# Kernel optimization log

Measured on AMD Instinct MI355X. Metric: run time of the kernel, lower is better.

The kernel has to match this reference:

```python
import jax, jax.numpy as jnp
import numpy as np

N_PRED = 10000
N_GT = 1000
NUM_CLASSES = 80
IMG_H = 800
IMG_W = 1333
EPS = 1e-12
ALPHA, GAMMA, CLS_W = 0.25, 2.0, 2.0
L1_W, IOU_W = 5.0, 2.0
CENTER_RADIUS = 2.5
CAND_TOPK = 5


def _make_boxes(key, n, w, h):
    k1, k2 = jax.random.split(key)
    cxcy = jax.random.uniform(k1, (n, 2)) * jnp.array([w, h], jnp.float32)
    wh = jax.random.uniform(k2, (n, 2)) * 190.0 + 10.0
    return jnp.concatenate([cxcy - wh / 2, cxcy + wh / 2], axis=1).astype(jnp.float32)


def setup_inputs() -> dict:
    key = jax.random.key(0)
    k1, k2, k3, k4 = jax.random.split(key, 4)
    return {
        'pred_logits': jax.random.normal(k1, (N_PRED, NUM_CLASSES), jnp.float32),
        'pred_boxes': _make_boxes(k2, N_PRED, IMG_W, IMG_H),
        'gt_bboxes': _make_boxes(k3, N_GT, IMG_W, IMG_H),
        'gt_labels': jax.random.randint(k4, (N_GT,), 0, NUM_CLASSES),
        'img_h': IMG_H,
        'img_w': IMG_W,
    }


def _pairwise_iou_giou(pred, gt):
    area_p = (pred[:, 2] - pred[:, 0]) * (pred[:, 3] - pred[:, 1])
    area_g = (gt[:, 2] - gt[:, 0]) * (gt[:, 3] - gt[:, 1])
    lt = jnp.maximum(pred[:, None, :2], gt[None, :, :2])
    rb = jnp.minimum(pred[:, None, 2:], gt[None, :, 2:])
    wh = jnp.clip(rb - lt, 0.0)
    inter = wh[..., 0] * wh[..., 1]                       # [N,G]
    union = area_p[:, None] + area_g[None, :] - inter
    iou = inter / jnp.maximum(union, EPS)
    elt = jnp.minimum(pred[:, None, :2], gt[None, :, :2])
    erb = jnp.maximum(pred[:, None, 2:], gt[None, :, 2:])
    ewh = jnp.clip(erb - elt, 0.0)
    enclose = ewh[..., 0] * ewh[..., 1]
    giou = iou - (enclose - union) / jnp.maximum(enclose, EPS)
    return iou, giou


def _center_info(pred, gt):
    # pred/gt in xyxy; uses pred box centers, strict inequalities as in source
    pcx = (pred[:, 0] + pred[:, 2]) * 0.5
    pcy = (pred[:, 1] + pred[:, 3]) * 0.5
    gx1, gy1, gx2, gy2 = gt[:, 0], gt[:, 1], gt[:, 2], gt[:, 3]
    in_boxes = ((pcx[:, None] > gx1) & (pcx[:, None] < gx2) &
                (pcy[:, None] > gy1) & (pcy[:, None] < gy2))
    gcx, gcy = (gx1 + gx2) * 0.5, (gy1 + gy2) * 0.5
    gw, gh = gx2 - gx1, gy2 - gy1
    r = CENTER_RADIUS
    in_centers = ((pcx[:, None] > gcx - r * gw) & (pcx[:, None] < gcx + r * gw) &
                  (pcy[:, None] > gcy - r * gh) & (pcy[:, None] < gcy + r * gh))
    valid = in_boxes.any(1) | in_centers.any(1)
    return valid, in_boxes & in_centers


def _compute_cost_and_ious(pred_logits, pred_boxes, gt_bboxes, gt_labels, img_h, img_w):
    # FocalLossCost
    p = jax.nn.sigmoid(pred_logits)
    neg = -jnp.log1p(-(p - EPS)) * (1 - ALPHA) * p ** GAMMA
    pos = -jnp.log(p + EPS) * ALPHA * (1 - p) ** GAMMA
    cls_cost = (pos - neg)[:, gt_labels] * CLS_W            # [N,G]
    # BBoxL1Cost (normalized by image size)
    factor = jnp.array([img_w, img_h, img_w, img_h], jnp.float32)
    l1_cost = jnp.sum(jnp.abs(pred_boxes[:, None, :] / factor -
                              gt_bboxes[None, :, :] / factor), -1) * L1_W
    # IoUCost (giou) + pairwise ious for dynamic-k
    ious, giou = _pairwise_iou_giou(pred_boxes, gt_bboxes)
    iou_cost = -giou * IOU_W
    valid_mask, in_boxes_and_center = _center_info(pred_boxes, gt_bboxes)
    cost = cls_cost + l1_cost + iou_cost + jnp.where(in_boxes_and_center, 0.0, 100.0)
    cost = cost + jnp.where(valid_mask, 0.0, 10000.0)[:, None]
    return cost, ious


def _dynamic_k_matching(cost, ious):
    n, g = cost.shape
    k = min(CAND_TOPK, n)
    topk_ious, _ = jax.lax.top_k(ious.T, k)                 # [G,k]
    dynamic_ks = jnp.maximum(topk_ious.sum(1).astype(jnp.int32), 1)
    _, idx = jax.lax.top_k(-cost.T, k)                      # [G,k] smallest costs per gt
    vals = (jnp.arange(k)[None, :] < dynamic_ks[:, None]).astype(cost.dtype)
    cols = jnp.broadcast_to(jnp.arange(g)[:, None], (g, k))
    mm = jnp.zeros_like(cost).at[idx, cols].max(vals)       # scatter 1s per gt column
    # resolve priors matched to >1 gt (note: mask is reused stale inside the loop, as in source)
    prior_mask = mm.sum(1) > 1
    cmin = jnp.argmin(cost, axis=1)
    mm = jnp.where(prior_mask[:, None], jax.nn.one_hot(cmin, g, dtype=cost.dtype), mm)

    def cond(state):
        m, _ = state
        return jnp.any(m.sum(0) == 0)

    def body(state):
        m, c = state
        matched_q = m.sum(1) > 0
        c = c + 100000.0 * matched_q[:, None].astype(c.dtype)
        unmatched = m.sum(0) == 0
        pos = jnp.argmin(c, axis=0)                         # [G]
        oh = jax.nn.one_hot(pos, n, dtype=c.dtype).T        # [N,G]
        m = jnp.where(unmatched[None, :], oh, m)
        cmin2 = jnp.argmin(c, axis=1)
        m_fix = jnp.where(prior_mask[:, None], jax.nn.one_hot(cmin2, g, dtype=c.dtype), m)
        m = jnp.where(jnp.any(m.sum(1) > 1), m_fix, m)
        return (m, c)

    mm, _ = jax.lax.while_loop(cond, body, (mm, cost))
    fg_mask = mm.sum(1) > 0
    matched = jnp.argmax(mm, axis=1).astype(jnp.int32)
    return fg_mask, jnp.where(fg_mask, matched, 0)


def reference(pred_logits, pred_boxes, gt_bboxes, gt_labels, img_h, img_w):
    cost, ious = _compute_cost_and_ious(pred_logits, pred_boxes, gt_bboxes,
                                        gt_labels, img_h, img_w)
    fg_mask, matched_gt = _dynamic_k_matching(cost, ious)
    # dense form: matched_gt[i] valid only where fg_mask[i] (fixed-shape version of
    # the original's compressed matched_gt_inds = mm[fg_mask].argmax(1))
    return fg_mask, matched_gt
```

## Files before the change

### kernel.cpp

```cpp
#include <hip/hip_runtime.h>
#include <cfloat>
#include <cmath>

#define NP 10000
#define NG 1000
#define NC 80
#define LMAX 6
#define NCH 2
#define CHSZ (NP / NCH)
#define MAIN_IT 19
#define TAIL_N  136

#define S_MULTI 12
#define S_BODY  16
#define RI_BIG  0x3fffffff
#define KMAX    0xFFFFFFFFFFFFFFFFull

#define TKEY    0xC248000000000000ull
#define CAND_CAP 1536

__device__ __forceinline__ bool lexless(float av, int ai, float bv, int bi) {
    return (av < bv) || (av == bv && ai < bi);
}

__device__ __forceinline__ unsigned long long packkey(float v, int idx) {
    unsigned u = __float_as_uint(v);
    u ^= (unsigned)(((int)u) >> 31) | 0x80000000u;
    return ((unsigned long long)u << 32) | (unsigned)idx;
}
__device__ __forceinline__ int keyidx(unsigned long long k) {
    return (int)(unsigned)(k & 0xFFFFFFFFu);
}

__device__ __forceinline__ float inflate(float c, int k) {
    for (int q = 0; q < k; q++) c += 100000.0f;
    return c;
}

__device__ __forceinline__ void cost_iou(float4 p, float4 pn, float4 pi,
        float4 g, float4 cb, float4 Gn, float ga, float clsv,
        float& cc_out, float& iou_out) {
#pragma clang fp contract(off)
    float wx = fminf(p.z, g.z) - fmaxf(p.x, g.x); wx = fmaxf(wx, 0.0f);
    float wy = fminf(p.w, g.w) - fmaxf(p.y, g.y); wy = fmaxf(wy, 0.0f);
    float inter = wx * wy;
    float uni = pi.z + ga - inter;
    float iou = inter / fmaxf(uni, 1e-12f);
    float ex = fmaxf(p.z, g.z) - fminf(p.x, g.x); ex = fmaxf(ex, 0.0f);
    float ey = fmaxf(p.w, g.w) - fminf(p.y, g.y); ey = fmaxf(ey, 0.0f);
    float enc = ex * ey;
    float giou = iou - (enc - uni) / fmaxf(enc, 1e-12f);
    float l1 = ((fabsf(pn.x - Gn.x) + fabsf(pn.y - Gn.y))
                + fabsf(pn.z - Gn.z)) + fabsf(pn.w - Gn.w);
    float cc = clsv + l1 * 5.0f;
    cc = cc + (-giou * 2.0f);
    bool inb = (pi.x > g.x && pi.x < g.z && pi.y > g.y && pi.y < g.w);
    bool inc = (pi.x > cb.x && pi.x < cb.z && pi.y > cb.y && pi.y < cb.w);
    cc = cc + ((inb && inc) ? 0.0f : 100.0f);
    cc = cc + pi.w;
    cc_out = cc; iou_out = iou;
}

#define CLS_TI 64
#define PB_CLS0 40
#define PB_G0   197
#define PB_V0   201
__global__ __launch_bounds__(256) void k_prep(const float* __restrict__ logits,
        const float* __restrict__ pb, const float* __restrict__ gb,
        const int* __restrict__ imgw, const int* __restrict__ imgh,
        float* __restrict__ clsval, float4* __restrict__ pnorm,
        float4* __restrict__ pinfo, float4* __restrict__ gcb,
        float4* __restrict__ gnm, float* __restrict__ gar,
        int* rowcnt, int* rowfirst, int* rowiter, int* prior, int* priorcol,
        int* colsum, int* scal)
{
    __shared__ float sl[CLS_TI * (NC + 1)];
    int b = blockIdx.x;
    if (b < PB_CLS0) {
        int i = b * 256 + threadIdx.x;
        if (i < NP) {
            rowcnt[i] = 0; rowfirst[i] = 0x7fffffff; rowiter[i] = RI_BIG;
            prior[i] = 0; priorcol[i] = 0;
        }
        if (i < NG) colsum[i] = 0;
        if (i < 32) scal[i] = 0;
    } else if (b < PB_G0) {
        int i0 = (b - PB_CLS0) * CLS_TI;
        bool full = (i0 + CLS_TI) <= NP;
        if (full) {
            const float* src = logits + (size_t)i0 * NC;
            for (int e = threadIdx.x; e < CLS_TI * NC; e += 256) {
                int di = e / NC, c = e - di * NC;
                sl[di * (NC + 1) + c] = src[e];
            }
        } else {
            for (int e = threadIdx.x; e < CLS_TI * NC; e += 256) {
                int di = e / NC, c = e - di * NC;
                int i = i0 + di;
                sl[di * (NC + 1) + c] = (i < NP) ? logits[(size_t)i * NC + c] : 0.0f;
            }
        }
        __syncthreads();
        for (int e = threadIdx.x; e < CLS_TI * NC; e += 256) {
            int c = e >> 6, di = e & 63;
            int i = i0 + di;
            if (i >= NP) continue;
            float x = sl[di * (NC + 1) + c];
            float p = 1.0f / (1.0f + expf(-x));
            float neg = -log1pf(-(p - 1e-12f)) * 0.75f * (p * p);
            float om = 1.0f - p;
            float pos = -logf(p + 1e-12f) * 0.25f * (om * om);
            clsval[(size_t)c * NP + i] = (pos - neg) * 2.0f;
        }
    } else if (b < PB_V0) {
#pragma clang fp contract(off)
        int j = (b - PB_G0) * 256 + threadIdx.x;
        if (j < NG) {
            float fw = (float)imgw[0], fh = (float)imgh[0];
            float4 g = ((const float4*)gb)[j];
            float gcx = (g.x + g.z) * 0.5f, gcy = (g.y + g.w) * 0.5f;
            float gw = g.z - g.x, gh = g.w - g.y;
            float4 cb; cb.x = gcx - 2.5f * gw; cb.y = gcy - 2.5f * gh;
            cb.z = gcx + 2.5f * gw; cb.w = gcy + 2.5f * gh;
            gcb[j] = cb;
            float4 Gn; Gn.x = g.x / fw; Gn.y = g.y / fh; Gn.z = g.z / fw; Gn.w = g.w / fh;
            gnm[j] = Gn;
            gar[j] = (g.z - g.x) * (g.w - g.y);
        }
    } else {
#pragma clang fp contract(off)
        int wave = threadIdx.x >> 6;
        int lane = threadIdx.x & 63;
        int i = (b - PB_V0) * 4 + wave;
        if (i >= NP) return;
        float4 p = ((const float4*)pb)[i];
        float pcx = (p.x + p.z) * 0.5f, pcy = (p.y + p.w) * 0.5f;
        int vb = 0, vc = 0;
        const float4* gb4 = (const float4*)gb;
        for (int jb = 0; jb < NG; jb += 64) {
            int j = jb + lane;
            if (j < NG) {
                float4 g = gb4[j];
                vb |= (pcx > g.x && pcx < g.z && pcy > g.y && pcy < g.w) ? 1 : 0;
                float gcx = (g.x + g.z) * 0.5f, gcy = (g.y + g.w) * 0.5f;
                float gw = g.z - g.x, gh = g.w - g.y;
                vc |= (pcx > gcx - 2.5f * gw && pcx < gcx + 2.5f * gw &&
                       pcy > gcy - 2.5f * gh && pcy < gcy + 2.5f * gh) ? 1 : 0;
            }
            if (__any(vb | vc)) break;
        }
        int any = __any(vb | vc) ? 1 : 0;
        if (lane == 0) {
            float fw = (float)imgw[0], fh = (float)imgh[0];
            float4 pn; pn.x = p.x / fw; pn.y = p.y / fh; pn.z = p.z / fw; pn.w = p.w / fh;
            pnorm[i] = pn;
            float4 pi4; pi4.x = pcx; pi4.y = pcy;
            pi4.z = (p.z - p.x) * (p.w - p.y);
            pi4.w = any ? 0.0f : 10000.0f;
            pinfo[i] = pi4;
        }
    }
}

__device__ __forceinline__ void upd2(unsigned long long& k0,
        unsigned long long& k1, unsigned long long key) {
    unsigned long long mx = (k0 > key) ? k0 : key;
    k0 = (k0 > key) ? key : k0;
    k1 = (k1 > mx) ? mx : k1;
}
__device__ __forceinline__ void updi2(float& i0, float& i1, float iou) {
    float mnv = fminf(i0, iou);
    i0 = fmaxf(i0, iou);
    i1 = fmaxf(i1, mnv);
}

__global__ __launch_bounds__(256) void k_cost2(
        const float* __restrict__ pb, const float* __restrict__ gb,
        const int* __restrict__ glab, const float* __restrict__ clsval,
        const float4* __restrict__ pnorm, const float4* __restrict__ pinfo,
        const float4* __restrict__ gcb, const float4* __restrict__ gnm,
        const float* __restrict__ gar,
        unsigned long long* __restrict__ pck, float* __restrict__ piv)
{
    __shared__ unsigned long long s_k[256 * 7];
    __shared__ float s_iv[256 * 7];
    __shared__ int s_bad;
    __shared__ int s_cnt;
    int* s_list = (int*)s_iv;

    int j = blockIdx.x >> 1;
    int c = blockIdx.x & 1;
    int tid = threadIdx.x;
    if (tid == 0) { s_bad = 0; s_cnt = 0; }
    float4 g  = ((const float4*)gb)[j];
    float4 cb = gcb[j];
    float4 Gn = gnm[j];
    float  ga = gar[j];
    const float* clscol = clsval + (size_t)glab[j] * NP;
    const float4* pb4 = (const float4*)pb;
    int base_i = c * CHSZ;
    __syncthreads();

    for (int k = 0; k <= MAIN_IT; k++) {
        if (k == MAIN_IT && tid >= TAIL_N) break;
        int i = base_i + tid + k * 256;
        float4 p = pb4[i];
        bool o = (p.z > g.x) & (g.z > p.x) & (p.w > g.y) & (g.w > p.y);
        unsigned long long m = __ballot(o ? 1 : 0);
        if (m) {
            int ln = tid & 63;
            int basew = 0;
            if (ln == 0) basew = atomicAdd(&s_cnt, __popcll(m));
            basew = __shfl(basew, 0);
            if (o) {
                int slot = basew + __popcll(m & ((1ull << ln) - 1ull));
                if (slot < CAND_CAP) s_list[slot] = i;
            }
        }
    }
    __syncthreads();
    int cnt = s_cnt;
    bool overflow = (cnt > CAND_CAP);
    if (overflow) cnt = 0;

    unsigned long long k0 = KMAX, k1 = KMAX;
    float i0 = 0.0f, i1 = 0.0f;
    for (int q = tid; q < cnt; q += 256) {
        int i = s_list[q];
        float cc, iou;
        cost_iou(pb4[i], pnorm[i], pinfo[i], g, cb, Gn, ga, clscol[i], cc, iou);
        upd2(k0, k1, packkey(cc, i));
        updi2(i0, i1, iou);
    }
    __syncthreads();

    int base = tid * 7;
    s_k[base+0] = k0; s_k[base+1] = k1;
    s_k[base+2] = KMAX; s_k[base+3] = KMAX; s_k[base+4] = KMAX; s_k[base+5] = KMAX;
    s_iv[base+0] = i0; s_iv[base+1] = i1;
    s_iv[base+2] = 0.0f; s_iv[base+3] = 0.0f; s_iv[base+4] = 0.0f; s_iv[base+5] = 0.0f;
    __syncthreads();

    for (int w = 128; w > 0; w >>= 1) {
        if (tid < w) {
            int a = tid * 7, bb = (tid + w) * 7;
            unsigned long long ok[5]; float og[5];
            int pa = a, pbp = bb;
#pragma unroll
            for (int t = 0; t < 5; t++) {
                unsigned long long A = s_k[pa], B = s_k[pbp];
                if (A <= B) { ok[t] = A; pa++; } else { ok[t] = B; pbp++; }
            }
            int qa = a, qb = bb;
#pragma unroll
            for (int t = 0; t < 5; t++) {
                float A = s_iv[qa], B = s_iv[qb];
                if (A >= B) { og[t] = A; qa++; } else { og[t] = B; qb++; }
            }
#pragma unroll
            for (int t = 0; t < 5; t++) { s_k[a+t] = ok[t]; s_iv[a+t] = og[t]; }
        }
        __syncthreads();
    }

    if (overflow || s_k[4] >= TKEY || k1 < s_k[4] || i1 > s_iv[4]) s_bad = 1;
    __syncthreads();

    if (s_bad) {
        unsigned long long kv[5]; float iv[5];
#pragma unroll
        for (int t = 0; t < 5; t++) { kv[t] = KMAX; iv[t] = -1.0f; }
        for (int k = 0; k <= MAIN_IT; k++) {
            if (k == MAIN_IT && tid >= TAIL_N) break;
            int i = base_i + tid + k * 256;
            float cc, iou;
            cost_iou(pb4[i], pnorm[i], pinfo[i], g, cb, Gn, ga, clscol[i], cc, iou);
            unsigned long long key = packkey(cc, i);
            if (key < kv[4]) {
                kv[4] = key;
#pragma unroll
                for (int t = 4; t > 0; t--)
                    if (kv[t] < kv[t-1]) { unsigned long long tv = kv[t]; kv[t] = kv[t-1]; kv[t-1] = tv; }
            }
            if (iou > iv[4]) {
                iv[4] = iou;
#pragma unroll
                for (int t = 4; t > 0; t--)
                    if (iv[t] > iv[t-1]) { float tv = iv[t]; iv[t] = iv[t-1]; iv[t-1] = tv; }
            }
        }
#pragma unroll
        for (int t = 0; t < 5; t++) { s_k[base+t] = kv[t]; s_iv[base+t] = iv[t]; }
        s_k[base+5] = KMAX; s_iv[base+5] = -2.0f;
        __syncthreads();
        for (int w = 128; w > 0; w >>= 1) {
            if (tid < w) {
                int a = tid * 7, bb = (tid + w) * 7;
                unsigned long long ok[5]; float og[5];
                int pa = a, pbp = bb;
#pragma unroll
                for (int t = 0; t < 5; t++) {
                    unsigned long long A = s_k[pa], B = s_k[pbp];
                    if (A <= B) { ok[t] = A; pa++; } else { ok[t] = B; pbp++; }
                }
                int qa = a, qb = bb;
#pragma unroll
                for (int t = 0; t < 5; t++) {
                    float A = s_iv[qa], B = s_iv[qb];
                    if (A >= B) { og[t] = A; qa++; } else { og[t] = B; qb++; }
                }
#pragma unroll
                for (int t = 0; t < 5; t++) { s_k[a+t] = ok[t]; s_iv[a+t] = og[t]; }
            }
            __syncthreads();
        }
    }

    if (tid == 0) {
        int ob = blockIdx.x * 5;
#pragma unroll
        for (int t = 0; t < 5; t++) { pck[ob + t] = s_k[t]; piv[ob + t] = s_iv[t]; }
    }
}

__global__ __launch_bounds__(256) void k_costmerge(
        const unsigned long long* __restrict__ pck, const float* __restrict__ piv,
        int* __restrict__ rowcnt, int* __restrict__ rowfirst,
        int* __restrict__ rowiter, int* __restrict__ top5,
        int* __restrict__ dkarr)
{
    int j = blockIdx.x * 256 + threadIdx.x;
    if (j >= NG) return;
    int base = j * 2 * 5;
    int h0 = 0, h1 = 0;
    int besti[5];
#pragma unroll
    for (int r = 0; r < 5; r++) {
        unsigned long long v0 = pck[base + h0];
        unsigned long long v1 = pck[base + 5 + h1];
        if (v0 <= v1) { besti[r] = keyidx(v0); h0++; }
        else          { besti[r] = keyidx(v1); h1++; }
    }
    int g0 = 0, g1 = 0;
    float ivm[5];
#pragma unroll
    for (int r = 0; r < 5; r++) {
        float v0 = piv[base + g0];
        float v1 = piv[base + 5 + g1];
        if (v0 >= v1) { ivm[r] = v0; g0++; } else { ivm[r] = v1; g1++; }
    }
    float s = (((ivm[0] + ivm[1]) + ivm[2]) + ivm[3]) + ivm[4];
    int dk = (int)s;
    if (dk < 1) dk = 1;
    dkarr[j] = dk;
#pragma unroll
    for (int r = 0; r < 5; r++) top5[j * 5 + r] = besti[r];
    for (int t = 0; t < dk; t++) {
        int r = besti[t];
        atomicAdd(&rowcnt[r], 1);
        atomicMin(&rowfirst[r], j);
        atomicMin(&rowiter[r], -1);
    }
}

__global__ __launch_bounds__(256) void k_pfixsurv(const float* __restrict__ pb,
        const float* __restrict__ gb, const int* __restrict__ glab,
        const float* __restrict__ clsval,
        const float4* __restrict__ pnorm, const float4* __restrict__ pinfo,
        const float4* __restrict__ gcb, const float4* __restrict__ gnm,
        const float* __restrict__ gar,
        int* __restrict__ prior, int* __restrict__ priorcol,
        int* __restrict__ colsum,
        const int* __restrict__ rowcnt, const int* __restrict__ top5,
        const int* __restrict__ dkarr)
{
    int b = blockIdx.x;
    int tid = threadIdx.x;
    if (b >= 2500) {
        int j = (b - 2500) * 256 + tid;
        if (j >= NG) return;
        int c = 0;
        int dk = dkarr[j];
        for (int t = 0; t < dk; t++) if (rowcnt[top5[j * 5 + t]] == 1) c++;
        if (c) atomicAdd(&colsum[j], c);
        return;
    }
    __shared__ float rv[256]; __shared__ int ri[256];
    for (int q = 0; q < 4; q++) {
        int row = b * 4 + q;
        if (rowcnt[row] <= 1) continue;
        if (tid == 0) prior[row] = 1;
        float4 p = ((const float4*)pb)[row];
        float4 pn = pnorm[row];
        float4 pi4 = pinfo[row];
        float best = FLT_MAX; int bj = 0x7fffffff;
        for (int j = tid; j < NG; j += 256) {
            float cc, iou;
            cost_iou(p, pn, pi4, ((const float4*)gb)[j], gcb[j], gnm[j], gar[j],
                     clsval[(size_t)glab[j] * NP + row], cc, iou);
            if (lexless(cc, j, best, bj)) { best = cc; bj = j; }
        }
        rv[tid] = best; ri[tid] = bj; __syncthreads();
        for (int w = 128; w > 0; w >>= 1) {
            if (tid < w) {
                float ov = rv[tid + w]; int oi = ri[tid + w];
                if (lexless(ov, oi, rv[tid], ri[tid])) { rv[tid] = ov; ri[tid] = oi; }
            }
            __syncthreads();
        }
        if (tid == 0) {
            priorcol[row] = ri[0];
            atomicAdd(&colsum[ri[0]], 1);
        }
        __syncthreads();
    }
}

__global__ __launch_bounds__(256) void k_iterB(const float* __restrict__ pb,
        const float* __restrict__ gb, const int* __restrict__ glab,
        const float* __restrict__ clsval,
        const float4* __restrict__ pnorm, const float4* __restrict__ pinfo,
        const float4* __restrict__ gcb, const float4* __restrict__ gnm,
        const float* __restrict__ gar, const int* __restrict__ top5,
        int* __restrict__ rowiter, int* __restrict__ rowcnt,
        int* __restrict__ rowfirst, int* __restrict__ colsum,
        int* __restrict__ scal, int t)
{
    int j = blockIdx.x;
    if (colsum[j] != 0) return;
    int tid = threadIdx.x;
    if (tid == 0) scal[S_BODY + t] = 1;

    __shared__ int s_pos;
    if (tid == 0) {
        int pos = -1;
        for (int r = 0; r < 5; r++) {
            int i = top5[j * 5 + r];
            if (rowiter[i] >= t) { pos = i; break; }
        }
        s_pos = pos;
    }
    __syncthreads();
    int pos = s_pos;

    if (pos < 0) {
        float4 g  = ((const float4*)gb)[j];
        float4 cb = gcb[j];
        float4 Gn = gnm[j];
        float  ga = gar[j];
        const float* clscol = clsval + (size_t)glab[j] * NP;
        const float4* pb4 = (const float4*)pb;
        __shared__ float rv[256]; __shared__ int ri[256];
        float best = FLT_MAX; int bi = 0x7fffffff;
        for (int i = tid; i < NP; i += 256) {
            if (rowiter[i] < t) continue;
            float cc, iou;
            cost_iou(pb4[i], pnorm[i], pinfo[i], g, cb, Gn, ga, clscol[i], cc, iou);
            if (lexless(cc, i, best, bi)) { best = cc; bi = i; }
        }
        rv[tid] = best; ri[tid] = bi; __syncthreads();
        for (int w = 128; w > 0; w >>= 1) {
            if (tid < w) {
                float ov = rv[tid + w]; int oi = ri[tid + w];
                if (lexless(ov, oi, rv[tid], ri[tid])) { rv[tid] = ov; ri[tid] = oi; }
            }
            __syncthreads();
        }
        pos = ri[0];
    }

    if (tid == 0) {
        colsum[j] = 1;
        int old = atomicAdd(&rowcnt[pos], 1);
        if (old >= 1) scal[S_MULTI] = 1;
        atomicMin(&rowfirst[pos], j);
        atomicMin(&rowiter[pos], t);
    }
}

__global__ __launch_bounds__(256) void k_iterC(const float* __restrict__ pb,
        const float* __restrict__ gb, const int* __restrict__ glab,
        const float* __restrict__ clsval,
        const float4* __restrict__ pnorm, const float4* __restrict__ pinfo,
        const float4* __restrict__ gcb, const float4* __restrict__ gnm,
        const float* __restrict__ gar,
        const int* __restrict__ prior, const int* __restrict__ rowiter,
        int* __restrict__ priorcol, int* __restrict__ colsum,
        int* __restrict__ scal, int t)
{
    if (scal[S_BODY + t] == 0 || scal[S_MULTI] == 0) return;
    int b = blockIdx.x;
    int tid = threadIdx.x;
    __shared__ float rv[256]; __shared__ int ri[256];
    for (int q = 0; q < 4; q++) {
        int row = b * 4 + q;
        if (!prior[row]) continue;
        int k = t - rowiter[row]; if (k < 0) k = 0;
        float4 p = ((const float4*)pb)[row];
        float4 pn = pnorm[row];
        float4 pi4 = pinfo[row];
        float best = FLT_MAX; int bj = 0x7fffffff;
        for (int j = tid; j < NG; j += 256) {
            float cc, iou;
            cost_iou(p, pn, pi4, ((const float4*)gb)[j], gcb[j], gnm[j], gar[j],
                     clsval[(size_t)glab[j] * NP + row], cc, iou);
            float val = inflate(cc, k);
            if (lexless(val, j, best, bj)) { best = val; bj = j; }
        }
        rv[tid] = best; ri[tid] = bj; __syncthreads();
        for (int w = 128; w > 0; w >>= 1) {
            if (tid < w) {
                float ov = rv[tid + w]; int oi = ri[tid + w];
                if (lexless(ov, oi, rv[tid], ri[tid])) { rv[tid] = ov; ri[tid] = oi; }
            }
            __syncthreads();
        }
        if (tid == 0) {
            int nb = ri[0];
            int oldc = priorcol[row];
            if (nb != oldc) {
                atomicSub(&colsum[oldc], 1);
                atomicAdd(&colsum[nb], 1);
                priorcol[row] = nb;
            }
        }
        __syncthreads();
    }
}

__global__ __launch_bounds__(256) void k_final(const int* __restrict__ rowcnt,
        const int* __restrict__ prior, const int* __restrict__ priorcol,
        const int* __restrict__ rowfirst, int* __restrict__ out)
{
    int i = blockIdx.x * 256 + threadIdx.x;
    if (i >= NP) return;
    int fg = rowcnt[i] > 0;
    out[i] = fg ? 1 : 0;
    out[NP + i] = fg ? (prior[i] ? priorcol[i] : rowfirst[i]) : 0;
}

extern "C" void kernel_launch(void* const* d_in, const int* in_sizes, int n_in,
                              void* d_out, int out_size, void* d_ws, size_t ws_size,
                              hipStream_t stream)
{
    (void)in_sizes; (void)n_in; (void)out_size; (void)ws_size;
    const float* logits = (const float*)d_in[0];
    const float* pboxes = (const float*)d_in[1];
    const float* gboxes = (const float*)d_in[2];
    const int*   glab   = (const int*)d_in[3];
    const int*   imgh   = (const int*)d_in[4];
    const int*   imgw   = (const int*)d_in[5];
    int* out = (int*)d_out;

    char* w = (char*)d_ws;
    float*  clsval  = (float*)(w);
    float4* pnorm   = (float4*)(w + 3200000);
    float4* pinfo   = (float4*)(w + 3360000);
    float4* gcb     = (float4*)(w + 3520000);
    float4* gnm     = (float4*)(w + 3536000);
    float*  gar     = (float*)(w + 3552000);
    int* rowcnt     = (int*)(w + 3556000);
    int* rowfirst   = (int*)(w + 3596000);
    int* rowiter    = (int*)(w + 3636000);
    int* prior      = (int*)(w + 3676000);
    int* priorcol   = (int*)(w + 3716000);
    int* top5       = (int*)(w + 3756000);
    int* dkarr      = (int*)(w + 3776000);
    int* colsum     = (int*)(w + 3780000);
    int* scal       = (int*)(w + 3784000);
    unsigned long long* pck = (unsigned long long*)(w + 3784128);
    float* piv      = (float*)(w + 3864128);

    hipLaunchKernelGGL(k_prep, dim3(2701), dim3(256), 0, stream,
                       logits, pboxes, gboxes, imgw, imgh,
                       clsval, pnorm, pinfo, gcb, gnm, gar,
                       rowcnt, rowfirst, rowiter, prior, priorcol, colsum, scal);
    hipLaunchKernelGGL(k_cost2, dim3(NG * NCH), dim3(256), 0, stream,
                       pboxes, gboxes, glab, clsval, pnorm, pinfo, gcb, gnm, gar,
                       pck, piv);
    hipLaunchKernelGGL(k_costmerge, dim3(4), dim3(256), 0, stream,
                       pck, piv, rowcnt, rowfirst, rowiter, top5, dkarr);
    hipLaunchKernelGGL(k_pfixsurv, dim3(2504), dim3(256), 0, stream,
                       pboxes, gboxes, glab, clsval, pnorm, pinfo, gcb, gnm, gar,
                       prior, priorcol, colsum, rowcnt, top5, dkarr);
    for (int t = 0; t < LMAX; t++) {
        hipLaunchKernelGGL(k_iterB, dim3(NG), dim3(256), 0, stream,
                           pboxes, gboxes, glab, clsval, pnorm, pinfo, gcb, gnm, gar,
                           top5, rowiter, rowcnt, rowfirst, colsum, scal, t);
        hipLaunchKernelGGL(k_iterC, dim3(2500), dim3(256), 0, stream,
                           pboxes, gboxes, glab, clsval, pnorm, pinfo, gcb, gnm, gar,
                           prior, rowiter, priorcol, colsum, scal, t);
    }
    hipLaunchKernelGGL(k_final, dim3(40), dim3(256), 0, stream,
                       rowcnt, prior, priorcol, rowfirst, out);
}
```

Before: 158.7 us.

## Build per-GT candidate lists in separate scatter kernel and fuse cost merge

Candidate pred-GT overlap detection moves out of the per-GT cost kernel into a new scatter kernel. It tiles 50 GT boxes in shared memory and appends overlapping pred indices to global per-GT lists using atomics. The cost kernel then runs one block per GT over that list, keeps a full top-5 per thread, and writes top-k, dynamic-k and row atomics directly, so the separate merge kernel is removed. This trades the per-block full scan of 10000 preds for an extra launch, global atomics and list traffic, with a full-scan fallback when a list overflows or lacks enough finite keys.

```diff
diff --git a/kernel.cpp b/kernel.cpp
--- a/kernel.cpp
+++ b/kernel.cpp
@@ -6,10 +6,6 @@
 #define NG 1000
 #define NC 80
 #define LMAX 6
-#define NCH 2
-#define CHSZ (NP / NCH)
-#define MAIN_IT 19
-#define TAIL_N  136
 
 #define S_MULTI 12
 #define S_BODY  16
@@ -17,7 +13,14 @@
 #define KMAX    0xFFFFFFFFFFFFFFFFull
 
 #define TKEY    0xC248000000000000ull
-#define CAND_CAP 1536
+
+#define CAP     1024
+#define CMAIN   39
+#define CTAIL   16
+
+#define GTILE   50
+#define NGTILES 20
+#define PBLKS   40
 
 __device__ __forceinline__ bool lexless(float av, int ai, float bv, int bi) {
     return (av < bv) || (av == bv && ai < bi);
@@ -61,6 +64,24 @@
     cc_out = cc; iou_out = iou;
 }
 
+__device__ __forceinline__ void ins5k(unsigned long long* kv,
+        unsigned long long key) {
+    if (key < kv[4]) {
+        kv[4] = key;
+#pragma unroll
+        for (int t = 4; t > 0; t--)
+            if (kv[t] < kv[t-1]) { unsigned long long tv = kv[t]; kv[t] = kv[t-1]; kv[t-1] = tv; }
+    }
+}
+__device__ __forceinline__ void ins5i(float* iv, float iou) {
+    if (iou > iv[4]) {
+        iv[4] = iou;
+#pragma unroll
+        for (int t = 4; t > 0; t--)
+            if (iv[t] > iv[t-1]) { float tv = iv[t]; iv[t] = iv[t-1]; iv[t-1] = tv; }
+    }
+}
+
 #define CLS_TI 64
 #define PB_CLS0 40
 #define PB_G0   197
@@ -72,7 +93,7 @@
         float4* __restrict__ pinfo, float4* __restrict__ gcb,
         float4* __restrict__ gnm, float* __restrict__ gar,
         int* rowcnt, int* rowfirst, int* rowiter, int* prior, int* priorcol,
-        int* colsum, int* scal)
+        int* colsum, int* scal, int* candcnt)
 {
     __shared__ float sl[CLS_TI * (NC + 1)];
     int b = blockIdx.x;
@@ -82,7 +103,7 @@
             rowcnt[i] = 0; rowfirst[i] = 0x7fffffff; rowiter[i] = RI_BIG;
             prior[i] = 0; priorcol[i] = 0;
         }
-        if (i < NG) colsum[i] = 0;
+        if (i < NG) { colsum[i] = 0; candcnt[i] = 0; }
         if (i < 32) scal[i] = 0;
     } else if (b < PB_G0) {
         int i0 = (b - PB_CLS0) * CLS_TI;
@@ -162,16 +183,54 @@
     }
 }
 
-__device__ __forceinline__ void upd2(unsigned long long& k0,
-        unsigned long long& k1, unsigned long long key) {
-    unsigned long long mx = (k0 > key) ? k0 : key;
-    k0 = (k0 > key) ? key : k0;
-    k1 = (k1 > mx) ? mx : k1;
-}
-__device__ __forceinline__ void updi2(float& i0, float& i1, float iou) {
-    float mnv = fminf(i0, iou);
-    i0 = fmaxf(i0, iou);
-    i1 = fmaxf(i1, mnv);
+__global__ __launch_bounds__(256) void k_scatter(const float* __restrict__ pb,
+        const float* __restrict__ gb, int* __restrict__ candcnt,
+        int* __restrict__ candlist)
+{
+    __shared__ float4 sg[GTILE];
+    int pblk = blockIdx.x / NGTILES;
+    int gt0  = (blockIdx.x - pblk * NGTILES) * GTILE;
+    int tid = threadIdx.x;
+    if (tid < GTILE) sg[tid] = ((const float4*)gb)[gt0 + tid];
+    __syncthreads();
+    int i = pblk * 256 + tid;
+    bool live = (i < NP);
+    float4 p = live ? ((const float4*)pb)[i]
+                    : float4{-1e30f, -1e30f, -1e30f, -1e30f};
+    for (int q = 0; q < GTILE; q++) {
+        float4 gq = sg[q];
+        bool o = (p.z > gq.x) & (gq.z > p.x) & (p.w > gq.y) & (gq.w > p.y);
+        if (o) {
+            int j = gt0 + q;
+            int slot = atomicAdd(&candcnt[j], 1);
+            if (slot < CAP) candlist[(size_t)j * CAP + slot] = i;
+        }
+    }
+}
+
+__device__ __forceinline__ void tree57(unsigned long long* s_k, float* s_iv,
+        int tid) {
+    for (int w = 128; w > 0; w >>= 1) {
+        if (tid < w) {
+            int a = tid * 7, bb = (tid + w) * 7;
+            unsigned long long ok[5]; float og[5];
+            int pa = a, pbp = bb;
+#pragma unroll
+            for (int t = 0; t < 5; t++) {
+                unsigned long long A = s_k[pa], B = s_k[pbp];
+                if (A <= B) { ok[t] = A; pa++; } else { ok[t] = B; pbp++; }
+            }
+            int qa = a, qb = bb;
+#pragma unroll
+            for (int t = 0; t < 5; t++) {
+                float A = s_iv[qa], B = s_iv[qb];
+                if (A >= B) { og[t] = A; qa++; } else { og[t] = B; qb++; }
+            }
+#pragma unroll
+            for (int t = 0; t < 5; t++) { s_k[a+t] = ok[t]; s_iv[a+t] = og[t]; }
+        }
+        __syncthreads();
+    }
 }
 
 __global__ __launch_bounds__(256) void k_cost2(
@@ -180,186 +239,94 @@
         const float4* __restrict__ pnorm, const float4* __restrict__ pinfo,
         const float4* __restrict__ gcb, const float4* __restrict__ gnm,
         const float* __restrict__ gar,
-        unsigned long long* __restrict__ pck, float* __restrict__ piv)
+        const int* __restrict__ candcnt, const int* __restrict__ candlist,
+        int* __restrict__ rowcnt, int* __restrict__ rowfirst,
+        int* __restrict__ rowiter, int* __restrict__ top5,
+        int* __restrict__ dkarr)
 {
     __shared__ unsigned long long s_k[256 * 7];
     __shared__ float s_iv[256 * 7];
-    __shared__ int s_bad;
-    __shared__ int s_cnt;
-    int* s_list = (int*)s_iv;
-
-    int j = blockIdx.x >> 1;
-    int c = blockIdx.x & 1;
+
+    int j = blockIdx.x;
     int tid = threadIdx.x;
-    if (tid == 0) { s_bad = 0; s_cnt = 0; }
     float4 g  = ((const float4*)gb)[j];
     float4 cb = gcb[j];
     float4 Gn = gnm[j];
     float  ga = gar[j];
     const float* clscol = clsval + (size_t)glab[j] * NP;
     const float4* pb4 = (const float4*)pb;
-    int base_i = c * CHSZ;
-    __syncthreads();
-
-    for (int k = 0; k <= MAIN_IT; k++) {
-        if (k == MAIN_IT && tid >= TAIL_N) break;
-        int i = base_i + tid + k * 256;
-        float4 p = pb4[i];
-        bool o = (p.z > g.x) & (g.z > p.x) & (p.w > g.y) & (g.w > p.y);
-        unsigned long long m = __ballot(o ? 1 : 0);
-        if (m) {
-            int ln = tid & 63;
-            int basew = 0;
-            if (ln == 0) basew = atomicAdd(&s_cnt, __popcll(m));
-            basew = __shfl(basew, 0);
-            if (o) {
-                int slot = basew + __popcll(m & ((1ull << ln) - 1ull));
-                if (slot < CAND_CAP) s_list[slot] = i;
-            }
-        }
-    }
-    __syncthreads();
-    int cnt = s_cnt;
-    bool overflow = (cnt > CAND_CAP);
-    if (overflow) cnt = 0;
-
-    unsigned long long k0 = KMAX, k1 = KMAX;
-    float i0 = 0.0f, i1 = 0.0f;
-    for (int q = tid; q < cnt; q += 256) {
-        int i = s_list[q];
-        float cc, iou;
-        cost_iou(pb4[i], pnorm[i], pinfo[i], g, cb, Gn, ga, clscol[i], cc, iou);
-        upd2(k0, k1, packkey(cc, i));
-        updi2(i0, i1, iou);
-    }
-    __syncthreads();
-
-    int base = tid * 7;
-    s_k[base+0] = k0; s_k[base+1] = k1;
-    s_k[base+2] = KMAX; s_k[base+3] = KMAX; s_k[base+4] = KMAX; s_k[base+5] = KMAX;
-    s_iv[base+0] = i0; s_iv[base+1] = i1;
-    s_iv[base+2] = 0.0f; s_iv[base+3] = 0.0f; s_iv[base+4] = 0.0f; s_iv[base+5] = 0.0f;
-    __syncthreads();
-
-    for (int w = 128; w > 0; w >>= 1) {
-        if (tid < w) {
-            int a = tid * 7, bb = (tid + w) * 7;
-            unsigned long long ok[5]; float og[5];
-            int pa = a, pbp = bb;
-#pragma unroll
-            for (int t = 0; t < 5; t++) {
-                unsigned long long A = s_k[pa], B = s_k[pbp];
-                if (A <= B) { ok[t] = A; pa++; } else { ok[t] = B; pbp++; }
-            }
-            int qa = a, qb = bb;
-#pragma unroll
-            for (int t = 0; t < 5; t++) {
-                float A = s_iv[qa], B = s_iv[qb];
-                if (A >= B) { og[t] = A; qa++; } else { og[t] = B; qb++; }
-            }
-#pragma unroll
-            for (int t = 0; t < 5; t++) { s_k[a+t] = ok[t]; s_iv[a+t] = og[t]; }
-        }
-        __syncthreads();
-    }
-
-    if (overflow || s_k[4] >= TKEY || k1 < s_k[4] || i1 > s_iv[4]) s_bad = 1;
-    __syncthreads();
-
-    if (s_bad) {
-        unsigned long long kv[5]; float iv[5];
-#pragma unroll
-        for (int t = 0; t < 5; t++) { kv[t] = KMAX; iv[t] = -1.0f; }
-        for (int k = 0; k <= MAIN_IT; k++) {
-            if (k == MAIN_IT && tid >= TAIL_N) break;
-            int i = base_i + tid + k * 256;
+
+    int cnt = candcnt[j];
+    bool dense = (cnt <= CAP);
+
+    unsigned long long kv[5]; float iv[5];
+#pragma unroll
+    for (int t = 0; t < 5; t++) { kv[t] = KMAX; iv[t] = dense ? 0.0f : -1.0f; }
+
+    if (dense) {
+        const int* lst = candlist + (size_t)j * CAP;
+        for (int q = tid; q < cnt; q += 256) {
+            int i = lst[q];
             float cc, iou;
             cost_iou(pb4[i], pnorm[i], pinfo[i], g, cb, Gn, ga, clscol[i], cc, iou);
-            unsigned long long key = packkey(cc, i);
-            if (key < kv[4]) {
-                kv[4] = key;
-#pragma unroll
-                for (int t = 4; t > 0; t--)
-                    if (kv[t] < kv[t-1]) { unsigned long long tv = kv[t]; kv[t] = kv[t-1]; kv[t-1] = tv; }
-            }
-            if (iou > iv[4]) {
-                iv[4] = iou;
-#pragma unroll
-                for (int t = 4; t > 0; t--)
-                    if (iv[t] > iv[t-1]) { float tv = iv[t]; iv[t] = iv[t-1]; iv[t-1] = tv; }
-            }
+            ins5k(kv, packkey(cc, i));
+            ins5i(iv, iou);
+        }
+    } else {
+        for (int k = 0; k <= CMAIN; k++) {
+            if (k == CMAIN && tid >= CTAIL) break;
+            int i = tid + k * 256;
+            float cc, iou;
+            cost_iou(pb4[i], pnorm[i], pinfo[i], g, cb, Gn, ga, clscol[i], cc, iou);
+            ins5k(kv, packkey(cc, i));
+            ins5i(iv, iou);
+        }
+    }
+
+    int base = tid * 7;
+#pragma unroll
+    for (int t = 0; t < 5; t++) { s_k[base+t] = kv[t]; s_iv[base+t] = iv[t]; }
+    s_k[base+5] = KMAX; s_iv[base+5] = -2.0f;
+    __syncthreads();
+    tree57(s_k, s_iv, tid);
+
+    bool redo = dense && (s_k[4] >= TKEY);
+    __syncthreads();
+
+    if (redo) {
+#pragma unroll
+        for (int t = 0; t < 5; t++) { kv[t] = KMAX; iv[t] = -1.0f; }
+        for (int k = 0; k <= CMAIN; k++) {
+            if (k == CMAIN && tid >= CTAIL) break;
+            int i = tid + k * 256;
+            float cc, iou;
+            cost_iou(pb4[i], pnorm[i], pinfo[i], g, cb, Gn, ga, clscol[i], cc, iou);
+            ins5k(kv, packkey(cc, i));
+            ins5i(iv, iou);
         }
 #pragma unroll
         for (int t = 0; t < 5; t++) { s_k[base+t] = kv[t]; s_iv[base+t] = iv[t]; }
         s_k[base+5] = KMAX; s_iv[base+5] = -2.0f;
         __syncthreads();
-        for (int w = 128; w > 0; w >>= 1) {
-            if (tid < w) {
-                int a = tid * 7, bb = (tid + w) * 7;
-                unsigned long long ok[5]; float og[5];
-                int pa = a, pbp = bb;
-#pragma unroll
-                for (int t = 0; t < 5; t++) {
-                    unsigned long long A = s_k[pa], B = s_k[pbp];
-                    if (A <= B) { ok[t] = A; pa++; } else { ok[t] = B; pbp++; }
-                }
-                int qa = a, qb = bb;
-#pragma unroll
-                for (int t = 0; t < 5; t++) {
-                    float A = s_iv[qa], B = s_iv[qb];
-                    if (A >= B) { og[t] = A; qa++; } else { og[t] = B; qb++; }
-                }
-#pragma unroll
-                for (int t = 0; t < 5; t++) { s_k[a+t] = ok[t]; s_iv[a+t] = og[t]; }
-            }
-            __syncthreads();
-        }
+        tree57(s_k, s_iv, tid);
     }
 
     if (tid == 0) {
-        int ob = blockIdx.x * 5;
-#pragma unroll
-        for (int t = 0; t < 5; t++) { pck[ob + t] = s_k[t]; piv[ob + t] = s_iv[t]; }
-    }
-}
-
-__global__ __launch_bounds__(256) void k_costmerge(
-        const unsigned long long* __restrict__ pck, const float* __restrict__ piv,
-        int* __restrict__ rowcnt, int* __restrict__ rowfirst,
-        int* __restrict__ rowiter, int* __restrict__ top5,
-        int* __restrict__ dkarr)
-{
-    int j = blockIdx.x * 256 + threadIdx.x;
-    if (j >= NG) return;
-    int base = j * 2 * 5;
-    int h0 = 0, h1 = 0;
-    int besti[5];
-#pragma unroll
-    for (int r = 0; r < 5; r++) {
-        unsigned long long v0 = pck[base + h0];
-        unsigned long long v1 = pck[base + 5 + h1];
-        if (v0 <= v1) { besti[r] = keyidx(v0); h0++; }
-        else          { besti[r] = keyidx(v1); h1++; }
-    }
-    int g0 = 0, g1 = 0;
-    float ivm[5];
-#pragma unroll
-    for (int r = 0; r < 5; r++) {
-        float v0 = piv[base + g0];
-        float v1 = piv[base + 5 + g1];
-        if (v0 >= v1) { ivm[r] = v0; g0++; } else { ivm[r] = v1; g1++; }
-    }
-    float s = (((ivm[0] + ivm[1]) + ivm[2]) + ivm[3]) + ivm[4];
-    int dk = (int)s;
-    if (dk < 1) dk = 1;
-    dkarr[j] = dk;
-#pragma unroll
-    for (int r = 0; r < 5; r++) top5[j * 5 + r] = besti[r];
-    for (int t = 0; t < dk; t++) {
-        int r = besti[t];
-        atomicAdd(&rowcnt[r], 1);
-        atomicMin(&rowfirst[r], j);
-        atomicMin(&rowiter[r], -1);
+        float s = (((s_iv[0] + s_iv[1]) + s_iv[2]) + s_iv[3]) + s_iv[4];
+        int dk = (int)s;
+        if (dk < 1) dk = 1;
+        dkarr[j] = dk;
+#pragma unroll
+        for (int t = 0; t < 5; t++) top5[j * 5 + t] = keyidx(s_k[t]);
+#pragma unroll
+        for (int t = 0; t < 5; t++) {
+            if (t < dk) {
+                int r = keyidx(s_k[t]);
+                atomicAdd(&rowcnt[r], 1);
+                atomicMin(&rowfirst[r], j);
+                atomicMin(&rowiter[r], -1);
+            }
+        }
     }
 }
 
@@ -568,18 +535,20 @@
     int* dkarr      = (int*)(w + 3776000);
     int* colsum     = (int*)(w + 3780000);
     int* scal       = (int*)(w + 3784000);
-    unsigned long long* pck = (unsigned long long*)(w + 3784128);
-    float* piv      = (float*)(w + 3864128);
+    int* candcnt    = (int*)(w + 3784128);
+    int* candlist   = (int*)(w + 3788128);
 
     hipLaunchKernelGGL(k_prep, dim3(2701), dim3(256), 0, stream,
                        logits, pboxes, gboxes, imgw, imgh,
                        clsval, pnorm, pinfo, gcb, gnm, gar,
-                       rowcnt, rowfirst, rowiter, prior, priorcol, colsum, scal);
-    hipLaunchKernelGGL(k_cost2, dim3(NG * NCH), dim3(256), 0, stream,
+                       rowcnt, rowfirst, rowiter, prior, priorcol, colsum, scal,
+                       candcnt);
+    hipLaunchKernelGGL(k_scatter, dim3(PBLKS * NGTILES), dim3(256), 0, stream,
+                       pboxes, gboxes, candcnt, candlist);
+    hipLaunchKernelGGL(k_cost2, dim3(NG), dim3(256), 0, stream,
                        pboxes, gboxes, glab, clsval, pnorm, pinfo, gcb, gnm, gar,
-                       pck, piv);
-    hipLaunchKernelGGL(k_costmerge, dim3(4), dim3(256), 0, stream,
-                       pck, piv, rowcnt, rowfirst, rowiter, top5, dkarr);
+                       candcnt, candlist,
+                       rowcnt, rowfirst, rowiter, top5, dkarr);
     hipLaunchKernelGGL(k_pfixsurv, dim3(2504), dim3(256), 0, stream,
                        pboxes, gboxes, glab, clsval, pnorm, pinfo, gcb, gnm, gar,
                        prior, priorcol, colsum, rowcnt, top5, dkarr);
```

Result: slower. 221.8 us (+39.8%).
